# Optimization experiments

Measured on AMD Instinct MI355X. Metric: run time of the kernel, lower is better.

## Reference

```python
import math
import jax, jax.numpy as jnp
import numpy as np

WINDOW = 2  # LocalAttention default window_size
EPS = 1e-6


def _linear(x, W, b):
    return x @ W + b


def local_attention(x, Wq, bq, Wk, bk, Wv, bv):
    # x: [B, S, D]
    B, S, D = x.shape
    q = _linear(x, Wq, bq)
    k = _linear(x, Wk, bk)
    v = _linear(x, Wv, bv)
    idx = jnp.arange(S)
    # 0/1 banded mask -> softmax gives a dense row-stochastic matrix (faithful to source)
    mask = (jnp.abs(idx[:, None] - idx[None, :]) <= WINDOW).astype(x.dtype)  # [S, S]
    A = jax.nn.softmax(mask, axis=-1)  # [S, S]
    kk = jnp.einsum('st,btd->bsd', A, k)  # bmm(A, k)
    scores = jnp.einsum('bsd,btd->bst', q, kk) / math.sqrt(D)
    return jnp.einsum('bst,btd->bsd', jax.nn.softmax(scores, axis=-1), v)


def whole_norm(x, w, b):
    # LayerNorm with normalized_shape == full [B, S, D]: normalize over ALL elements
    mu = jnp.mean(x)
    var = jnp.mean(jnp.square(x - mu))
    return (x - mu) * jax.lax.rsqrt(var + EPS) * w + b


def ffn(x, W1, b1, W2, b2):
    return _linear(jax.nn.relu(_linear(x, W1, b1)), W2, b2)


def branch(feat, Wq, bq, Wk, bk, Wv, bv, W1, b1, W2, b2, nw, nb):
    out = local_attention(feat, Wq, bq, Wk, bk, Wv, bv)
    out = whole_norm(out + feat, nw, nb)
    out = ffn(out, W1, b1, W2, b2)
    return whole_norm(out + feat, nw, nb)


def _make_params(key, B, S, D):
    ks = jax.random.split(key, 5)
    s = 1.0 / math.sqrt(D)
    Wq = jax.random.normal(ks[0], (D, D), jnp.float32) * s
    Wk = jax.random.normal(ks[1], (D, D), jnp.float32) * s
    Wv = jax.random.normal(ks[2], (D, D), jnp.float32) * s
    W1 = jax.random.normal(ks[3], (D, 4 * D), jnp.float32) * s
    W2 = jax.random.normal(ks[4], (4 * D, D), jnp.float32) * (1.0 / math.sqrt(4 * D))
    return dict(Wq=Wq, bq=jnp.zeros((D,)), Wk=Wk, bk=jnp.zeros((D,)),
                Wv=Wv, bv=jnp.zeros((D,)), W1=W1, b1=jnp.zeros((4 * D,)),
                W2=W2, b2=jnp.zeros((D,)), nw=jnp.ones((B, S, D)), nb=jnp.zeros((B, S, D)))


def setup_inputs() -> dict:
    key = jax.random.key(0)
    k0, k1, k2, k3 = jax.random.split(key, 4)
    B, St, Dt = 8, 512, 1024
    Si, Di = 196, 768
    inp = {
        'text_feature': jax.random.normal(k0, (B, St, Dt), jnp.float32),
        'image_feature': jax.random.normal(k1, (B, Si, Di), jnp.float32),
    }
    tp = _make_params(k2, B, St, Dt)
    ip = _make_params(k3, B, Si, Di)
    for k, v in tp.items():
        inp['t_' + k] = v
    for k, v in ip.items():
        inp['i_' + k] = v
    return inp


def reference(text_feature, image_feature,
              t_Wq, t_bq, t_Wk, t_bk, t_Wv, t_bv, t_W1, t_b1, t_W2, t_b2, t_nw, t_nb,
              i_Wq, i_bq, i_Wk, i_bk, i_Wv, i_bv, i_W1, i_b1, i_W2, i_b2, i_nw, i_nb):
    image_out = branch(image_feature, i_Wq, i_bq, i_Wk, i_bk, i_Wv, i_bv,
                       i_W1, i_b1, i_W2, i_b2, i_nw, i_nb)
    text_out = branch(text_feature, t_Wq, t_bq, t_Wk, t_bk, t_Wv, t_bv,
                      t_W1, t_b1, t_W2, t_b2, t_nw, t_nb)
    return (text_out, image_out)
```

## Files before the change

kernel.cpp:

```cpp
#include <hip/hip_runtime.h>
#include <math.h>

typedef float  f32x4  __attribute__((ext_vector_type(4)));
typedef short  bf16x8 __attribute__((ext_vector_type(8)));

__device__ __forceinline__ unsigned short f2bf(float f) {
    union { float f; unsigned u; } v; v.f = f;
    unsigned u = v.u;
    return (unsigned short)((u + 0x7FFFu + ((u >> 16) & 1u)) >> 16);
}
__device__ __forceinline__ float bf2f(unsigned short u) {
    union { unsigned u; float f; } v; v.u = (unsigned)u << 16; return v.f;
}

#define GLOAD_LDS16(g, l)                                                      \
    __builtin_amdgcn_global_load_lds(                                          \
        (const __attribute__((address_space(1))) void*)(g),                    \
        (__attribute__((address_space(3))) void*)(l), 16, 0, 0)

template<int BM, int BN, bool OUT_BF16, bool RELU>
__global__ __launch_bounds__(256)
void gemm_bf16(const unsigned short* __restrict__ A,
               const unsigned short* __restrict__ BT,
               const float* __restrict__ bias, void* __restrict__ Cv,
               int M, int N, int K, int lda, int ldb, int ldc,
               long long sA, long long sB, long long sC, float alpha,
               int gx, int gy)
{
    constexpr int BK = 32;
    constexpr int WM = BM / 2, WN = BN / 2;
    constexpr int MR = WM / 16, NR = WN / 16;
    __shared__ unsigned short Asm[BM * BK];
    __shared__ unsigned short Bsm[BN * BK];

    A  += (long long)blockIdx.z * sA;
    BT += (long long)blockIdx.z * sB;
    char* Cb = (char*)Cv + (long long)blockIdx.z * sC * (OUT_BF16 ? 2 : 4);

    const int nwg = gx * gy;
    {
        int orig = blockIdx.x;
        int xcd = orig & 7, sidx = orig >> 3;
        int qq = nwg >> 3, rr = nwg & 7;
        int wg = (xcd < rr ? xcd * (qq + 1) : rr * (qq + 1) + (xcd - rr) * qq) + sidx;
        (void)wg;
        const int by = wg % gy;
        const int bx = wg / gy;
        __shared__ int rc[2];
        if (threadIdx.x == 0) { rc[0] = by * BM; rc[1] = bx * BN; }
        __syncthreads();
    }
    int orig = blockIdx.x;
    int xcd = orig & 7, sidx = orig >> 3;
    int qq = nwg >> 3, rr = nwg & 7;
    int wg = (xcd < rr ? xcd * (qq + 1) : rr * (qq + 1) + (xcd - rr) * qq) + sidx;
    const int row0 = (wg % gy) * BM;
    const int col0 = (wg / gy) * BN;

    const int tid  = threadIdx.x;
    const int lane = tid & 63;
    const int wave = tid >> 6;
    const int wr   = wave >> 1;
    const int wc   = wave & 1;

    const int srow = tid >> 2;
    const int skel = (tid & 3) * 8;

    f32x4 acc[MR][NR] = {};

    const int lrow = lane & 15;
    const int lk   = (lane >> 4) * 8;

    for (int k0 = 0; k0 < K; k0 += BK) {
        #pragma unroll
        for (int is = 0; is < BM / 64; ++is) {
            const unsigned short* g =
                A + (long long)(row0 + is * 64 + srow) * lda + (k0 + skel);
            GLOAD_LDS16(g, &Asm[(is * 64 + srow) * BK + skel]);
        }
        #pragma unroll
        for (int is = 0; is < BN / 64; ++is) {
            const unsigned short* g =
                BT + (long long)(col0 + is * 64 + srow) * ldb + (k0 + skel);
            GLOAD_LDS16(g, &Bsm[(is * 64 + srow) * BK + skel]);
        }
        __syncthreads();

        bf16x8 af[MR], bfr[NR];
        #pragma unroll
        for (int mf = 0; mf < MR; ++mf)
            af[mf] = *(const bf16x8*)&Asm[(wr * WM + mf * 16 + lrow) * BK + lk];
        #pragma unroll
        for (int nf = 0; nf < NR; ++nf)
            bfr[nf] = *(const bf16x8*)&Bsm[(wc * WN + nf * 16 + lrow) * BK + lk];
        #pragma unroll
        for (int mf = 0; mf < MR; ++mf)
            #pragma unroll
            for (int nf = 0; nf < NR; ++nf)
                acc[mf][nf] = __builtin_amdgcn_mfma_f32_16x16x32_bf16(
                    af[mf], bfr[nf], acc[mf][nf], 0, 0, 0);
        __syncthreads();
    }

    const int crow = (lane >> 4) * 4;
    const int ccol = lane & 15;
    #pragma unroll
    for (int mf = 0; mf < MR; ++mf) {
        int rbase = row0 + wr * WM + mf * 16 + crow;
        #pragma unroll
        for (int nf = 0; nf < NR; ++nf) {
            int c = col0 + wc * WN + nf * 16 + ccol;
            if (c >= N) continue;
            float bv = bias ? bias[c] : 0.f;
            #pragma unroll
            for (int j = 0; j < 4; ++j) {
                int r = rbase + j;
                if (r >= M) continue;
                float v = acc[mf][nf][j] * alpha + bv;
                if (RELU) v = fmaxf(v, 0.f);
                if (OUT_BF16)
                    ((unsigned short*)Cb)[(long long)r * ldc + c] = f2bf(v);
                else
                    ((float*)Cb)[(long long)r * ldc + c] = v;
            }
        }
    }
}

template<int BM, int BN>
static void gemm_t(bool outBf16, bool relu,
                   const unsigned short* A, const unsigned short* BT, const float* bias,
                   void* C, int M, int N, int K, int lda, int ldb, int ldc,
                   int batch, long long sA, long long sB, long long sC,
                   float alpha, hipStream_t st)
{
    int gx = (N + BN - 1) / BN, gy = (M + BM - 1) / BM;
    dim3 grid(gx * gy, 1, batch);
    if (outBf16) {
        if (relu) gemm_bf16<BM, BN, true , true ><<<grid, 256, 0, st>>>(A, BT, bias, C, M, N, K, lda, ldb, ldc, sA, sB, sC, alpha, gx, gy);
        else      gemm_bf16<BM, BN, true , false><<<grid, 256, 0, st>>>(A, BT, bias, C, M, N, K, lda, ldb, ldc, sA, sB, sC, alpha, gx, gy);
    } else {
        if (relu) gemm_bf16<BM, BN, false, true ><<<grid, 256, 0, st>>>(A, BT, bias, C, M, N, K, lda, ldb, ldc, sA, sB, sC, alpha, gx, gy);
        else      gemm_bf16<BM, BN, false, false><<<grid, 256, 0, st>>>(A, BT, bias, C, M, N, K, lda, ldb, ldc, sA, sB, sC, alpha, gx, gy);
    }
}

__global__ void splitk_reduce_kernel(const float4* __restrict__ part,
                                     const float4* __restrict__ bias,
                                     float4* __restrict__ out,
                                     long long n4, int N4, int nsplit, long long stride4)
{
    long long i = (long long)blockIdx.x * blockDim.x + threadIdx.x;
    long long gs = (long long)gridDim.x * blockDim.x;
    for (; i < n4; i += gs) {
        float4 a = part[i];
        for (int s = 1; s < nsplit; ++s) {
            float4 b = part[(long long)s * stride4 + i];
            a.x += b.x; a.y += b.y; a.z += b.z; a.w += b.w;
        }
        float4 bv = bias[(int)(i % N4)];
        a.x += bv.x; a.y += bv.y; a.z += bv.z; a.w += bv.w;
        out[i] = a;
    }
}

__global__ void cast_bf16_kernel(const float4* __restrict__ in,
                                 ushort4* __restrict__ out, long long n4)
{
    long long i = (long long)blockIdx.x * blockDim.x + threadIdx.x;
    long long stride = (long long)gridDim.x * blockDim.x;
    for (; i < n4; i += stride) {
        float4 v = in[i];
        ushort4 o;
        o.x = f2bf(v.x); o.y = f2bf(v.y); o.z = f2bf(v.z); o.w = f2bf(v.w);
        out[i] = o;
    }
}

__global__ void transpose_cast_kernel(const float* __restrict__ src,
                                      unsigned short* __restrict__ dst,
                                      int R, int C, int Rpad,
                                      long long sSrc, long long sDst)
{
    __shared__ float t[32][33];
    src += (long long)blockIdx.z * sSrc;
    dst += (long long)blockIdx.z * sDst;
    int r0 = blockIdx.x * 32, c0 = blockIdx.y * 32;
    int tx = threadIdx.x & 31, ty = threadIdx.x >> 5;
    #pragma unroll
    for (int i = 0; i < 32; i += 8) {
        int r = r0 + ty + i, c = c0 + tx;
        t[ty + i][tx] = (r < R && c < C) ? src[(long long)r * C + c] : 0.f;
    }
    __syncthreads();
    #pragma unroll
    for (int i = 0; i < 32; i += 8) {
        int c = c0 + ty + i, r = r0 + tx;
        if (c < C && r < Rpad)
            dst[(long long)c * Rpad + r] = f2bf(t[tx][ty + i]);
    }
}

__global__ void transpose_bf16_kernel(const unsigned short* __restrict__ src,
                                      unsigned short* __restrict__ dst,
                                      int R, int C, int Rpad, int ldS,
                                      long long sSrc, long long sDst)
{
    __shared__ unsigned short t[32][33];
    src += (long long)blockIdx.z * sSrc;
    dst += (long long)blockIdx.z * sDst;
    int r0 = blockIdx.x * 32, c0 = blockIdx.y * 32;
    int tx = threadIdx.x & 31, ty = threadIdx.x >> 5;
    #pragma unroll
    for (int i = 0; i < 32; i += 8) {
        int r = r0 + ty + i, c = c0 + tx;
        t[ty + i][tx] = (r < R && c < C) ? src[(long long)r * ldS + c] : (unsigned short)0;
    }
    __syncthreads();
    #pragma unroll
    for (int i = 0; i < 32; i += 8) {
        int c = c0 + ty + i, r = r0 + tx;
        if (c < C && r < Rpad)
            dst[(long long)c * Rpad + r] = t[tx][ty + i];
    }
}

#define KTOT_NCH 16
__global__ void ktot_partial_bf16(const unsigned short* __restrict__ k,
                                  float* __restrict__ part,
                                  int B, int S, int D, int ld)
{
    int bch = blockIdx.x;
    int b  = bch / KTOT_NCH;
    int ch = bch % KTOT_NCH;
    int d  = blockIdx.y * 256 + threadIdx.x;
    if (d >= D) return;
    int len = (S + KTOT_NCH - 1) / KTOT_NCH;
    int lo = ch * len;
    int hi = lo + len < S ? lo + len : S;
    const unsigned short* kp = k + ((long long)b * S + lo) * ld + d;
    float s = 0.f;
    for (int t = lo; t < hi; ++t, kp += ld) s += bf2f(*kp);
    part[(long long)bch * D + d] = s;
}

__global__ void ktot_finish_kernel(const float* __restrict__ part,
                                   float* __restrict__ ktot, int B, int D)
{
    int idx = blockIdx.x * blockDim.x + threadIdx.x;
    if (idx >= B * D) return;
    int b = idx / D, d = idx % D;
    float s = 0.f;
    #pragma unroll
    for (int ch = 0; ch < KTOT_NCH; ++ch)
        s += part[((long long)b * KTOT_NCH + ch) * D + d];
    ktot[idx] = s;
}

__global__ void kk_bf16_kernel(const unsigned short* __restrict__ k,
                               const float* __restrict__ ktot,
                               unsigned short* __restrict__ kk,
                               int B, int S, int D, int ld)
{
    long long idx = (long long)blockIdx.x * blockDim.x + threadIdx.x;
    int D4 = D >> 2;
    long long n4 = (long long)B * S * D4;
    if (idx >= n4) return;
    int d4 = (int)(idx % D4);
    long long bs = idx / D4;
    int s = (int)(bs % S);
    int b = (int)(bs / S);
    int lo = s - 2 > 0 ? s - 2 : 0;
    int hi = s + 2 < S - 1 ? s + 2 : S - 1;
    int c = hi - lo + 1;
    const float E = 2.718281828459045f;
    float Zinv = 1.f / ((float)(S - c) + E * (float)c);

    float w0 = 0.f, w1 = 0.f, w2 = 0.f, w3 = 0.f;
    const unsigned short* kp = k + ((long long)b * S + lo) * ld + d4 * 4;
    for (int t = lo; t <= hi; ++t, kp += ld) {
        ushort4 kv = *(const ushort4*)kp;
        w0 += bf2f(kv.x); w1 += bf2f(kv.y); w2 += bf2f(kv.z); w3 += bf2f(kv.w);
    }
    float4 tot = *((const float4*)(ktot + b * D) + d4);
    ushort4 o;
    o.x = f2bf((tot.x + (E - 1.f) * w0) * Zinv);
    o.y = f2bf((tot.y + (E - 1.f) * w1) * Zinv);
    o.z = f2bf((tot.z + (E - 1.f) * w2) * Zinv);
    o.w = f2bf((tot.w + (E - 1.f) * w3) * Zinv);
    ((ushort4*)(kk + ((long long)b * S + s) * D))[d4] = o;
}

__global__ void softmax_rows_bf16(const float* __restrict__ sc,
                                  unsigned short* __restrict__ P, int S, int Spad)
{
    long long row = blockIdx.x;
    const float* p = sc + row * (long long)Spad;
    unsigned short* o = P + row * (long long)Spad;
    int tid = threadIdx.x;
    __shared__ float red[256];

    float m = -INFINITY;
    for (int t = tid; t < S; t += 256) m = fmaxf(m, p[t]);
    red[tid] = m; __syncthreads();
    for (int s = 128; s > 0; s >>= 1) {
        if (tid < s) red[tid] = fmaxf(red[tid], red[tid + s]);
        __syncthreads();
    }
    m = red[0];
    __syncthreads();

    float sum = 0.f;
    for (int t = tid; t < S; t += 256) sum += __expf(p[t] - m);
    red[tid] = sum; __syncthreads();
    for (int s = 128; s > 0; s >>= 1) {
        if (tid < s) red[tid] += red[tid + s];
        __syncthreads();
    }
    float inv = 1.f / red[0];
    for (int t = tid; t < Spad; t += 256)
        o[t] = (t < S) ? f2bf(__expf(p[t] - m) * inv) : (unsigned short)0;
}

__global__ void stats_kernel(const float4* __restrict__ a, const float4* __restrict__ f,
                             double* __restrict__ part, long long n4)
{
    __shared__ double rs[256], rs2[256];
    int tid = threadIdx.x;
    long long i = (long long)blockIdx.x * blockDim.x + tid;
    long long stride = (long long)gridDim.x * blockDim.x;
    double s = 0.0, s2 = 0.0;
    for (; i < n4; i += stride) {
        float4 av = a[i], fv = f[i];
        float z0 = av.x + fv.x, z1 = av.y + fv.y, z2 = av.z + fv.z, z3 = av.w + fv.w;
        s  += (double)z0 + (double)z1 + (double)z2 + (double)z3;
        s2 += (double)z0 * z0 + (double)z1 * z1 + (double)z2 * z2 + (double)z3 * z3;
    }
    rs[tid] = s; rs2[tid] = s2; __syncthreads();
    for (int k = 128; k > 0; k >>= 1) {
        if (tid < k) { rs[tid] += rs[tid + k]; rs2[tid] += rs2[tid + k]; }
        __syncthreads();
    }
    if (tid == 0) { part[2 * blockIdx.x] = rs[0]; part[2 * blockIdx.x + 1] = rs2[0]; }
}

__global__ void finish_stats(const double* __restrict__ part, int npart,
                             float* __restrict__ stats, double n)
{
    __shared__ double rs[256], rs2[256];
    int tid = threadIdx.x;
    double s = 0.0, s2 = 0.0;
    for (int i = tid; i < npart; i += 256) { s += part[2 * i]; s2 += part[2 * i + 1]; }
    rs[tid] = s; rs2[tid] = s2; __syncthreads();
    for (int k = 128; k > 0; k >>= 1) {
        if (tid < k) { rs[tid] += rs[tid + k]; rs2[tid] += rs2[tid + k]; }
        __syncthreads();
    }
    if (tid == 0) {
        double mu  = rs[0] / n;
        double var = rs2[0] / n - mu * mu;
        stats[0] = (float)mu;
        stats[1] = (float)(1.0 / sqrt(var + 1e-6));
    }
}

template<bool OUT_BF16>
__global__ void norm_apply_kernel(const float4* __restrict__ a, const float4* __restrict__ f,
                                  const float4* __restrict__ nw, const float4* __restrict__ nb,
                                  const float* __restrict__ stats, void* __restrict__ out,
                                  long long n4)
{
    float mu = stats[0], rstd = stats[1];
    long long i = (long long)blockIdx.x * blockDim.x + threadIdx.x;
    long long stride = (long long)gridDim.x * blockDim.x;
    for (; i < n4; i += stride) {
        float4 av = a[i], fv = f[i], wv = nw[i], bv = nb[i];
        float o0 = (av.x + fv.x - mu) * rstd * wv.x + bv.x;
        float o1 = (av.y + fv.y - mu) * rstd * wv.y + bv.y;
        float o2 = (av.z + fv.z - mu) * rstd * wv.z + bv.z;
        float o3 = (av.w + fv.w - mu) * rstd * wv.w + bv.w;
        if (OUT_BF16) {
            ushort4 o; o.x = f2bf(o0); o.y = f2bf(o1); o.z = f2bf(o2); o.w = f2bf(o3);
            ((ushort4*)out)[i] = o;
        } else {
            float4 o = {o0, o1, o2, o3};
            ((float4*)out)[i] = o;
        }
    }
}

struct Bufs {
    unsigned short *xb, *qkv, *kkb, *vT, *P, *h, *WqkvT, *W1T, *W2T;
    float *f32buf, *bqkv, *ktot, *ktot_part, *stats;
    double *part;
};

static void run_branch(const float* x, const float* const* w, bool big,
                       float* out, int B, int S, int D, const Bufs& wsb, hipStream_t st)
{
    const float *Wq = w[0], *bq = w[1], *Wk = w[2], *bk = w[3], *Wv = w[4], *bv = w[5];
    const float *W1 = w[6], *b1 = w[7], *W2 = w[8], *b2 = w[9], *nw = w[10], *nb = w[11];

    const int Spad = (S + 31) & ~31;
    const long long M = (long long)B * S;
    const long long n = M * D;
    const long long n4 = n / 4;
    const float inv_sqrt_d = (float)(1.0 / sqrt((double)D));
    const int D3 = 3 * D, D4 = 4 * D;

    unsigned short* y1b = wsb.kkb;
    float* scores = (float*)wsb.h;
    float* splitbuf = (float*)wsb.qkv;

    cast_bf16_kernel<<<1024, 256, 0, st>>>((const float4*)x, (ushort4*)wsb.xb, n4);
    transpose_cast_kernel<<<dim3((D + 31) / 32, (D + 31) / 32, 1), 256, 0, st>>>(Wq, wsb.WqkvT,            D, D, D, 0, 0);
    transpose_cast_kernel<<<dim3((D + 31) / 32, (D + 31) / 32, 1), 256, 0, st>>>(Wk, wsb.WqkvT + (long long)D * D,     D, D, D, 0, 0);
    transpose_cast_kernel<<<dim3((D + 31) / 32, (D + 31) / 32, 1), 256, 0, st>>>(Wv, wsb.WqkvT + 2LL * D * D, D, D, D, 0, 0);
    transpose_cast_kernel<<<dim3((D + 31) / 32, (D4 + 31) / 32, 1), 256, 0, st>>>(W1, wsb.W1T, D, D4, D, 0, 0);
    transpose_cast_kernel<<<dim3((D4 + 31) / 32, (D + 31) / 32, 1), 256, 0, st>>>(W2, wsb.W2T, D4, D, D4, 0, 0);
    hipMemcpyAsync(wsb.bqkv,         bq, D * sizeof(float), hipMemcpyDeviceToDevice, st);
    hipMemcpyAsync(wsb.bqkv + D,     bk, D * sizeof(float), hipMemcpyDeviceToDevice, st);
    hipMemcpyAsync(wsb.bqkv + 2 * D, bv, D * sizeof(float), hipMemcpyDeviceToDevice, st);

    if (big)
        gemm_t<128, 128>(true, false, wsb.xb, wsb.WqkvT, wsb.bqkv, wsb.qkv,
                         (int)M, D3, D, D, D, D3, 1, 0, 0, 0, 1.f, st);
    else
        gemm_t<128, 64>(true, false, wsb.xb, wsb.WqkvT, wsb.bqkv, wsb.qkv,
                        (int)M, D3, D, D, D, D3, 1, 0, 0, 0, 1.f, st);

    const unsigned short* kcol = wsb.qkv + D;
    ktot_partial_bf16<<<dim3(B * KTOT_NCH, (D + 255) / 256), 256, 0, st>>>(kcol, wsb.ktot_part, B, S, D, D3);
    ktot_finish_kernel<<<(B * D + 255) / 256, 256, 0, st>>>(wsb.ktot_part, wsb.ktot, B, D);
    kk_bf16_kernel<<<(int)((n4 + 255) / 256), 256, 0, st>>>(kcol, wsb.ktot, wsb.kkb, B, S, D, D3);

    transpose_bf16_kernel<<<dim3((Spad + 31) / 32, (D + 31) / 32, B), 256, 0, st>>>(
        wsb.qkv + 2 * D, wsb.vT, S, D, Spad, D3, (long long)S * D3, (long long)D * Spad);

    gemm_t<64, 64>(false, false, wsb.qkv, wsb.kkb, nullptr, scores, S, S, D, D3, D, Spad,
                   B, (long long)S * D3, (long long)S * D, (long long)S * Spad, inv_sqrt_d, st);
    softmax_rows_bf16<<<(int)M, 256, 0, st>>>(scores, wsb.P, S, Spad);

    gemm_t<128, 64>(false, false, wsb.P, wsb.vT, nullptr, wsb.f32buf, S, D, Spad, Spad, Spad, D,
                    B, (long long)S * Spad, (long long)D * Spad, (long long)S * D, 1.f, st);

    stats_kernel<<<1024, 256, 0, st>>>((const float4*)wsb.f32buf, (const float4*)x, wsb.part, n4);
    finish_stats<<<1, 256, 0, st>>>(wsb.part, 1024, wsb.stats, (double)n);
    norm_apply_kernel<true><<<2048, 256, 0, st>>>((const float4*)wsb.f32buf, (const float4*)x,
        (const float4*)nw, (const float4*)nb, wsb.stats, y1b, n4);

    if (big)
        gemm_t<128, 128>(true, true, y1b, wsb.W1T, b1, wsb.h, (int)M, D4, D, D, D, D4, 1, 0, 0, 0, 1.f, st);
    else
        gemm_t<128, 64>(true, true, y1b, wsb.W1T, b1, wsb.h, (int)M, D4, D, D, D, D4, 1, 0, 0, 0, 1.f, st);

    {
        int nsplit = big ? 2 : 4;
        int Ksp = D4 / nsplit;
        gemm_t<128, 64>(false, false, wsb.h, wsb.W2T, nullptr, splitbuf,
                        (int)M, D, Ksp, D4, D4, D,
                        nsplit, Ksp, Ksp, M * D, 1.f, st);
        splitk_reduce_kernel<<<2048, 256, 0, st>>>((const float4*)splitbuf, (const float4*)b2,
                                                   (float4*)wsb.f32buf, n4, D / 4, nsplit, n4);
    }

    stats_kernel<<<1024, 256, 0, st>>>((const float4*)wsb.f32buf, (const float4*)x, wsb.part, n4);
    finish_stats<<<1, 256, 0, st>>>(wsb.part, 1024, wsb.stats, (double)n);
    norm_apply_kernel<false><<<2048, 256, 0, st>>>((const float4*)wsb.f32buf, (const float4*)x,
        (const float4*)nw, (const float4*)nb, wsb.stats, out, n4);
}

extern "C" void kernel_launch(void* const* d_in, const int* in_sizes, int n_in,
                              void* d_out, int out_size, void* d_ws, size_t ws_size,
                              hipStream_t stream)
{
    const float* text  = (const float*)d_in[0];
    const float* image = (const float*)d_in[1];
    const float* tw[12];
    const float* iw[12];
    for (int i = 0; i < 12; ++i) tw[i] = (const float*)d_in[2 + i];
    for (int i = 0; i < 12; ++i) iw[i] = (const float*)d_in[14 + i];

    float* out_text = (float*)d_out;
    float* out_img  = out_text + 8LL * 512 * 1024;

    char* p = (char*)d_ws;
    auto alloc = [&](long long bytes) {
        char* r = p;
        p += (bytes + 255) & ~255LL;
        return r;
    };
    const long long MD  = 4096LL * 1024;
    const long long BDS = 8LL * 1024 * 512;
    const long long SS  = 8LL * 512 * 512;
    Bufs b;
    b.xb      = (unsigned short*)alloc(MD * 2);
    b.qkv     = (unsigned short*)alloc(MD * 3 * 2);
    b.kkb     = (unsigned short*)alloc(MD * 2);
    b.vT      = (unsigned short*)alloc(BDS * 2);
    b.P       = (unsigned short*)alloc(SS * 2);
    b.h       = (unsigned short*)alloc(MD * 4 * 2);
    b.WqkvT   = (unsigned short*)alloc(3LL * 1024 * 1024 * 2);
    b.W1T     = (unsigned short*)alloc(4096LL * 1024 * 2);
    b.W2T     = (unsigned short*)alloc(4096LL * 1024 * 2);
    b.f32buf  = (float*)alloc(MD * 4);
    b.bqkv    = (float*)alloc(3LL * 1024 * 4);
    b.ktot    = (float*)alloc(8192LL * 4);
    b.ktot_part = (float*)alloc(8192LL * KTOT_NCH * 4);
    b.part    = (double*)alloc(2048LL * 8);
    b.stats   = (float*)alloc(256);

    run_branch(text,  tw, true,  out_text, 8, 512, 1024, b, stream);
    run_branch(image, iw, false, out_img,  8, 196, 768,  b, stream);
}
```

Baseline: 522.4 us.

## Add double-buffered 8-wave GEMM for projections and fuse split-K reduce with norm stats

Adds a new GEMM kernel with 512 threads (8 waves in a 2x4 arrangement), double-buffered LDS tiles and a single barrier per K step, so global-to-LDS loads for the next tile overlap MFMA work on the current one. It is used for the QKV, FFN1 and FFN2 projections with larger tiles on the big branch. The split-K reduction now also adds the residual and accumulates the whole-tensor sum and sum of squares, which removes one full read pass before the final norm. The costs are higher LDS use per block and different occupancy, plus a barrier-free window between staging the next tile and reading the current one.

```diff
diff --git a/kernel.cpp b/kernel.cpp
--- a/kernel.cpp
+++ b/kernel.cpp
@@ -18,38 +18,26 @@
         (const __attribute__((address_space(1))) void*)(g),                    \
         (__attribute__((address_space(3))) void*)(l), 16, 0, 0)
 
-template<int BM, int BN, bool OUT_BF16, bool RELU>
-__global__ __launch_bounds__(256)
-void gemm_bf16(const unsigned short* __restrict__ A,
-               const unsigned short* __restrict__ BT,
-               const float* __restrict__ bias, void* __restrict__ Cv,
-               int M, int N, int K, int lda, int ldb, int ldc,
-               long long sA, long long sB, long long sC, float alpha,
-               int gx, int gy)
+template<int MR, int NR, bool OUT_BF16, bool RELU>
+__global__ __launch_bounds__(512, 2)
+void gemm2_bf16(const unsigned short* __restrict__ A,
+                const unsigned short* __restrict__ BT,
+                const float* __restrict__ bias, void* __restrict__ Cv,
+                int M, int N, int K, int lda, int ldb, int ldc,
+                long long sA, long long sB, long long sC, float alpha,
+                int gx, int gy)
 {
     constexpr int BK = 32;
-    constexpr int WM = BM / 2, WN = BN / 2;
-    constexpr int MR = WM / 16, NR = WN / 16;
-    __shared__ unsigned short Asm[BM * BK];
-    __shared__ unsigned short Bsm[BN * BK];
+    constexpr int WM = MR * 16, WN = NR * 16;
+    constexpr int BM = 2 * WM, BN = 4 * WN;
+    __shared__ unsigned short Asm[2][BM * BK];
+    __shared__ unsigned short Bsm[2][BN * BK];
 
     A  += (long long)blockIdx.z * sA;
     BT += (long long)blockIdx.z * sB;
     char* Cb = (char*)Cv + (long long)blockIdx.z * sC * (OUT_BF16 ? 2 : 4);
 
     const int nwg = gx * gy;
-    {
-        int orig = blockIdx.x;
-        int xcd = orig & 7, sidx = orig >> 3;
-        int qq = nwg >> 3, rr = nwg & 7;
-        int wg = (xcd < rr ? xcd * (qq + 1) : rr * (qq + 1) + (xcd - rr) * qq) + sidx;
-        (void)wg;
-        const int by = wg % gy;
-        const int bx = wg / gy;
-        __shared__ int rc[2];
-        if (threadIdx.x == 0) { rc[0] = by * BM; rc[1] = bx * BN; }
-        __syncthreads();
-    }
     int orig = blockIdx.x;
     int xcd = orig & 7, sidx = orig >> 3;
     int qq = nwg >> 3, rr = nwg & 7;
@@ -60,46 +48,51 @@
     const int tid  = threadIdx.x;
     const int lane = tid & 63;
     const int wave = tid >> 6;
-    const int wr   = wave >> 1;
-    const int wc   = wave & 1;
+    const int wr   = wave >> 2;
+    const int wc   = wave & 3;
 
     const int srow = tid >> 2;
     const int skel = (tid & 3) * 8;
 
-    f32x4 acc[MR][NR] = {};
-
     const int lrow = lane & 15;
     const int lk   = (lane >> 4) * 8;
 
-    for (int k0 = 0; k0 < K; k0 += BK) {
-        #pragma unroll
-        for (int is = 0; is < BM / 64; ++is) {
-            const unsigned short* g =
-                A + (long long)(row0 + is * 64 + srow) * lda + (k0 + skel);
-            GLOAD_LDS16(g, &Asm[(is * 64 + srow) * BK + skel]);
-        }
-        #pragma unroll
-        for (int is = 0; is < BN / 64; ++is) {
-            const unsigned short* g =
-                BT + (long long)(col0 + is * 64 + srow) * ldb + (k0 + skel);
-            GLOAD_LDS16(g, &Bsm[(is * 64 + srow) * BK + skel]);
-        }
-        __syncthreads();
+    f32x4 acc[MR][NR] = {};
+
+    auto stage = [&](int buf, int k0) {
+        #pragma unroll
+        for (int is = 0; is < BM / 128; ++is)
+            GLOAD_LDS16(A + (long long)(row0 + is * 128 + srow) * lda + (k0 + skel),
+                        &Asm[buf][(is * 128 + srow) * BK + skel]);
+        #pragma unroll
+        for (int is = 0; is < BN / 128; ++is)
+            GLOAD_LDS16(BT + (long long)(col0 + is * 128 + srow) * ldb + (k0 + skel),
+                        &Bsm[buf][(is * 128 + srow) * BK + skel]);
+    };
+
+    const int nt = K / BK;
+    stage(0, 0);
+    __syncthreads();
+    int cur = 0;
+    for (int t = 0; t < nt; ++t) {
+        if (t + 1 < nt) stage(cur ^ 1, (t + 1) * BK);
 
         bf16x8 af[MR], bfr[NR];
         #pragma unroll
         for (int mf = 0; mf < MR; ++mf)
-            af[mf] = *(const bf16x8*)&Asm[(wr * WM + mf * 16 + lrow) * BK + lk];
+            af[mf] = *(const bf16x8*)&Asm[cur][(wr * WM + mf * 16 + lrow) * BK + lk];
         #pragma unroll
         for (int nf = 0; nf < NR; ++nf)
-            bfr[nf] = *(const bf16x8*)&Bsm[(wc * WN + nf * 16 + lrow) * BK + lk];
+            bfr[nf] = *(const bf16x8*)&Bsm[cur][(wc * WN + nf * 16 + lrow) * BK + lk];
         #pragma unroll
         for (int mf = 0; mf < MR; ++mf)
             #pragma unroll
             for (int nf = 0; nf < NR; ++nf)
                 acc[mf][nf] = __builtin_amdgcn_mfma_f32_16x16x32_bf16(
                     af[mf], bfr[nf], acc[mf][nf], 0, 0, 0);
-        __syncthreads();
+
+        __syncthreads();
+        cur ^= 1;
     }
 
     const int crow = (lane >> 4) * 4;
@@ -127,8 +120,119 @@
     }
 }
 
+template<int MR, int NR>
+static void gemm2_t(bool outBf16, bool relu,
+                    const unsigned short* A, const unsigned short* BT, const float* bias,
+                    void* C, int M, int N, int K, int lda, int ldb, int ldc,
+                    int batch, long long sA, long long sB, long long sC,
+                    float alpha, hipStream_t st)
+{
+    const int BM = 2 * MR * 16, BN = 4 * NR * 16;
+    int gx = (N + BN - 1) / BN, gy = (M + BM - 1) / BM;
+    dim3 grid(gx * gy, 1, batch);
+    if (outBf16) {
+        if (relu) gemm2_bf16<MR, NR, true , true ><<<grid, 512, 0, st>>>(A, BT, bias, C, M, N, K, lda, ldb, ldc, sA, sB, sC, alpha, gx, gy);
+        else      gemm2_bf16<MR, NR, true , false><<<grid, 512, 0, st>>>(A, BT, bias, C, M, N, K, lda, ldb, ldc, sA, sB, sC, alpha, gx, gy);
+    } else {
+        if (relu) gemm2_bf16<MR, NR, false, true ><<<grid, 512, 0, st>>>(A, BT, bias, C, M, N, K, lda, ldb, ldc, sA, sB, sC, alpha, gx, gy);
+        else      gemm2_bf16<MR, NR, false, false><<<grid, 512, 0, st>>>(A, BT, bias, C, M, N, K, lda, ldb, ldc, sA, sB, sC, alpha, gx, gy);
+    }
+}
+
+template<int BM, int BN, bool OUT_BF16>
+__global__ __launch_bounds__(256)
+void gemm_bf16(const unsigned short* __restrict__ A,
+               const unsigned short* __restrict__ BT,
+               const float* __restrict__ bias, void* __restrict__ Cv,
+               int M, int N, int K, int lda, int ldb, int ldc,
+               long long sA, long long sB, long long sC, float alpha,
+               int gx, int gy)
+{
+    constexpr int BK = 32;
+    constexpr int WM = BM / 2, WN = BN / 2;
+    constexpr int MR = WM / 16, NR = WN / 16;
+    __shared__ unsigned short Asm[BM * BK];
+    __shared__ unsigned short Bsm[BN * BK];
+
+    A  += (long long)blockIdx.z * sA;
+    BT += (long long)blockIdx.z * sB;
+    char* Cb = (char*)Cv + (long long)blockIdx.z * sC * (OUT_BF16 ? 2 : 4);
+
+    const int nwg = gx * gy;
+    int orig = blockIdx.x;
+    int xcd = orig & 7, sidx = orig >> 3;
+    int qq = nwg >> 3, rr = nwg & 7;
+    int wg = (xcd < rr ? xcd * (qq + 1) : rr * (qq + 1) + (xcd - rr) * qq) + sidx;
+    const int row0 = (wg % gy) * BM;
+    const int col0 = (wg / gy) * BN;
+
+    const int tid  = threadIdx.x;
+    const int lane = tid & 63;
+    const int wave = tid >> 6;
+    const int wr   = wave >> 1;
+    const int wc   = wave & 1;
+
+    const int srow = tid >> 2;
+    const int skel = (tid & 3) * 8;
+
+    f32x4 acc[MR][NR] = {};
+
+    const int lrow = lane & 15;
+    const int lk   = (lane >> 4) * 8;
+
+    for (int k0 = 0; k0 < K; k0 += BK) {
+        #pragma unroll
+        for (int is = 0; is < BM / 64; ++is)
+            GLOAD_LDS16(A + (long long)(row0 + is * 64 + srow) * lda + (k0 + skel),
+                        &Asm[(is * 64 + srow) * BK + skel]);
+        #pragma unroll
+        for (int is = 0; is < BN / 64; ++is)
+            GLOAD_LDS16(BT + (long long)(col0 + is * 64 + srow) * ldb + (k0 + skel),
+                        &Bsm[(is * 64 + srow) * BK + skel]);
+        __syncthreads();
+
+        bf16x8 af[MR], bfr[NR];
+        #pragma unroll
+        for (int mf = 0; mf < MR; ++mf)
+            af[mf] = *(const bf16x8*)&Asm[(wr * WM + mf * 16 + lrow) * BK + lk];
+        #pragma unroll
+        for (int nf = 0; nf < NR; ++nf)
+            bfr[nf] = *(const bf16x8*)&Bsm[(wc * WN + nf * 16 + lrow) * BK + lk];
+        #pragma unroll
+        for (int mf = 0; mf < MR; ++mf)
+            #pragma unroll
+            for (int nf = 0; nf < NR; ++nf)
+                acc[mf][nf] = __builtin_amdgcn_mfma_f32_16x16x32_bf16(
+                    af[mf], bfr[nf], acc[mf][nf], 0, 0, 0);
+        __syncthreads();
+    }
+
+    const int crow = (lane >> 4) * 4;
+    const int ccol = lane & 15;
+    #pragma unroll
+    for (int mf = 0; mf < MR; ++mf) {
+        int rbase = row0 + wr * WM + mf * 16 + crow;
+        #pragma unroll
+        for (int nf = 0; nf < NR; ++nf) {
+            int c = col0 + wc * WN + nf * 16 + ccol;
+            if (c >= N) continue;
+            float bv = bias ? bias[c] : 0.f;
+            #pragma unroll
+            for (int j = 0; j < 4; ++j) {
+                int r = rbase + j;
+                if (r >= M) continue;
+                float v = acc[mf][nf][j] * alpha + bv;
+                if (OUT_BF16)
+                    ((unsigned short*)Cb)[(long long)r * ldc + c] = f2bf(v);
+                else
+                    ((float*)Cb)[(long long)r * ldc + c] = v;
+            }
+        }
+    }
+}
+
 template<int BM, int BN>
-static void gemm_t(bool outBf16, bool relu,
+static void gemm_t(bool outBf16,
                    const unsigned short* A, const unsigned short* BT, const float* bias,
                    void* C, int M, int N, int K, int lda, int ldb, int ldc,
                    int batch, long long sA, long long sB, long long sC,
@@ -136,31 +240,61 @@
 {
     int gx = (N + BN - 1) / BN, gy = (M + BM - 1) / BM;
     dim3 grid(gx * gy, 1, batch);
-    if (outBf16) {
-        if (relu) gemm_bf16<BM, BN, true , true ><<<grid, 256, 0, st>>>(A, BT, bias, C, M, N, K, lda, ldb, ldc, sA, sB, sC, alpha, gx, gy);
-        else      gemm_bf16<BM, BN, true , false><<<grid, 256, 0, st>>>(A, BT, bias, C, M, N, K, lda, ldb, ldc, sA, sB, sC, alpha, gx, gy);
-    } else {
-        if (relu) gemm_bf16<BM, BN, false, true ><<<grid, 256, 0, st>>>(A, BT, bias, C, M, N, K, lda, ldb, ldc, sA, sB, sC, alpha, gx, gy);
-        else      gemm_bf16<BM, BN, false, false><<<grid, 256, 0, st>>>(A, BT, bias, C, M, N, K, lda, ldb, ldc, sA, sB, sC, alpha, gx, gy);
-    }
-}
-
-__global__ void splitk_reduce_kernel(const float4* __restrict__ part,
-                                     const float4* __restrict__ bias,
-                                     float4* __restrict__ out,
-                                     long long n4, int N4, int nsplit, long long stride4)
-{
-    long long i = (long long)blockIdx.x * blockDim.x + threadIdx.x;
+    if (outBf16)
+        gemm_bf16<BM, BN, true ><<<grid, 256, 0, st>>>(A, BT, bias, C, M, N, K, lda, ldb, ldc, sA, sB, sC, alpha, gx, gy);
+    else
+        gemm_bf16<BM, BN, false><<<grid, 256, 0, st>>>(A, BT, bias, C, M, N, K, lda, ldb, ldc, sA, sB, sC, alpha, gx, gy);
+}
+
+__global__ void splitk_stats_kernel(const float4* __restrict__ part,
+                                    const float4* __restrict__ bias,
+                                    const float4* __restrict__ x,
+                                    float4* __restrict__ z,
+                                    double* __restrict__ dpart,
+                                    long long n4, int N4, int nsplit, long long stride4)
+{
+    __shared__ double rs[256], rs2[256];
+    int tid = threadIdx.x;
+    long long i = (long long)blockIdx.x * blockDim.x + tid;
     long long gs = (long long)gridDim.x * blockDim.x;
+    double s = 0.0, s2 = 0.0;
     for (; i < n4; i += gs) {
         float4 a = part[i];
-        for (int s = 1; s < nsplit; ++s) {
-            float4 b = part[(long long)s * stride4 + i];
+        for (int sp = 1; sp < nsplit; ++sp) {
+            float4 b = part[(long long)sp * stride4 + i];
             a.x += b.x; a.y += b.y; a.z += b.z; a.w += b.w;
         }
         float4 bv = bias[(int)(i % N4)];
-        a.x += bv.x; a.y += bv.y; a.z += bv.z; a.w += bv.w;
-        out[i] = a;
+        float4 xv = x[i];
+        a.x += bv.x + xv.x; a.y += bv.y + xv.y; a.z += bv.z + xv.z; a.w += bv.w + xv.w;
+        z[i] = a;
+        s  += (double)a.x + (double)a.y + (double)a.z + (double)a.w;
+        s2 += (double)a.x * a.x + (double)a.y * a.y + (double)a.z * a.z + (double)a.w * a.w;
+    }
+    rs[tid] = s; rs2[tid] = s2; __syncthreads();
+    for (int k = 128; k > 0; k >>= 1) {
+        if (tid < k) { rs[tid] += rs[tid + k]; rs2[tid] += rs2[tid + k]; }
+        __syncthreads();
+    }
+    if (tid == 0) { dpart[2 * blockIdx.x] = rs[0]; dpart[2 * blockIdx.x + 1] = rs2[0]; }
+}
+
+__global__ void norm_apply_z_kernel(const float4* __restrict__ z,
+                                    const float4* __restrict__ nw, const float4* __restrict__ nb,
+                                    const float* __restrict__ stats, float4* __restrict__ out,
+                                    long long n4)
+{
+    float mu = stats[0], rstd = stats[1];
+    long long i = (long long)blockIdx.x * blockDim.x + threadIdx.x;
+    long long stride = (long long)gridDim.x * blockDim.x;
+    for (; i < n4; i += stride) {
+        float4 zv = z[i], wv = nw[i], bv = nb[i];
+        float4 o;
+        o.x = (zv.x - mu) * rstd * wv.x + bv.x;
+        o.y = (zv.y - mu) * rstd * wv.y + bv.y;
+        o.z = (zv.z - mu) * rstd * wv.z + bv.z;
+        o.w = (zv.w - mu) * rstd * wv.w + bv.w;
+        out[i] = o;
     }
 }
 
@@ -364,10 +498,9 @@
     }
 }
 
-template<bool OUT_BF16>
 __global__ void norm_apply_kernel(const float4* __restrict__ a, const float4* __restrict__ f,
                                   const float4* __restrict__ nw, const float4* __restrict__ nb,
-                                  const float* __restrict__ stats, void* __restrict__ out,
+                                  const float* __restrict__ stats, ushort4* __restrict__ out,
                                   long long n4)
 {
     float mu = stats[0], rstd = stats[1];
@@ -375,17 +508,12 @@
     long long stride = (long long)gridDim.x * blockDim.x;
     for (; i < n4; i += stride) {
         float4 av = a[i], fv = f[i], wv = nw[i], bv = nb[i];
-        float o0 = (av.x + fv.x - mu) * rstd * wv.x + bv.x;
-        float o1 = (av.y + fv.y - mu) * rstd * wv.y + bv.y;
-        float o2 = (av.z + fv.z - mu) * rstd * wv.z + bv.z;
-        float o3 = (av.w + fv.w - mu) * rstd * wv.w + bv.w;
-        if (OUT_BF16) {
-            ushort4 o; o.x = f2bf(o0); o.y = f2bf(o1); o.z = f2bf(o2); o.w = f2bf(o3);
-            ((ushort4*)out)[i] = o;
-        } else {
-            float4 o = {o0, o1, o2, o3};
-            ((float4*)out)[i] = o;
-        }
+        ushort4 o;
+        o.x = f2bf((av.x + fv.x - mu) * rstd * wv.x + bv.x);
+        o.y = f2bf((av.y + fv.y - mu) * rstd * wv.y + bv.y);
+        o.z = f2bf((av.z + fv.z - mu) * rstd * wv.z + bv.z);
+        o.w = f2bf((av.w + fv.w - mu) * rstd * wv.w + bv.w);
+        out[i] = o;
     }
 }
 
@@ -413,8 +541,8 @@
     float* splitbuf = (float*)wsb.qkv;
 
     cast_bf16_kernel<<<1024, 256, 0, st>>>((const float4*)x, (ushort4*)wsb.xb, n4);
-    transpose_cast_kernel<<<dim3((D + 31) / 32, (D + 31) / 32, 1), 256, 0, st>>>(Wq, wsb.WqkvT,            D, D, D, 0, 0);
-    transpose_cast_kernel<<<dim3((D + 31) / 32, (D + 31) / 32, 1), 256, 0, st>>>(Wk, wsb.WqkvT + (long long)D * D,     D, D, D, 0, 0);
+    transpose_cast_kernel<<<dim3((D + 31) / 32, (D + 31) / 32, 1), 256, 0, st>>>(Wq, wsb.WqkvT,               D, D, D, 0, 0);
+    transpose_cast_kernel<<<dim3((D + 31) / 32, (D + 31) / 32, 1), 256, 0, st>>>(Wk, wsb.WqkvT + (long long)D * D, D, D, D, 0, 0);
     transpose_cast_kernel<<<dim3((D + 31) / 32, (D + 31) / 32, 1), 256, 0, st>>>(Wv, wsb.WqkvT + 2LL * D * D, D, D, D, 0, 0);
     transpose_cast_kernel<<<dim3((D + 31) / 32, (D4 + 31) / 32, 1), 256, 0, st>>>(W1, wsb.W1T, D, D4, D, 0, 0);
     transpose_cast_kernel<<<dim3((D4 + 31) / 32, (D + 31) / 32, 1), 256, 0, st>>>(W2, wsb.W2T, D4, D, D4, 0, 0);
@@ -423,11 +551,11 @@
     hipMemcpyAsync(wsb.bqkv + 2 * D, bv, D * sizeof(float), hipMemcpyDeviceToDevice, st);
 
     if (big)
-        gemm_t<128, 128>(true, false, wsb.xb, wsb.WqkvT, wsb.bqkv, wsb.qkv,
-                         (int)M, D3, D, D, D, D3, 1, 0, 0, 0, 1.f, st);
+        gemm2_t<8, 2>(true, false, wsb.xb, wsb.WqkvT, wsb.bqkv, wsb.qkv,
+                      (int)M, D3, D, D, D, D3, 1, 0, 0, 0, 1.f, st);
     else
-        gemm_t<128, 64>(true, false, wsb.xb, wsb.WqkvT, wsb.bqkv, wsb.qkv,
-                        (int)M, D3, D, D, D, D3, 1, 0, 0, 0, 1.f, st);
+        gemm2_t<4, 2>(true, false, wsb.xb, wsb.WqkvT, wsb.bqkv, wsb.qkv,
+                      (int)M, D3, D, D, D, D3, 1, 0, 0, 0, 1.f, st);
 
     const unsigned short* kcol = wsb.qkv + D;
     ktot_partial_bf16<<<dim3(B * KTOT_NCH, (D + 255) / 256), 256, 0, st>>>(kcol, wsb.ktot_part, B, S, D, D3);
@@ -437,37 +565,41 @@
     transpose_bf16_kernel<<<dim3((Spad + 31) / 32, (D + 31) / 32, B), 256, 0, st>>>(
         wsb.qkv + 2 * D, wsb.vT, S, D, Spad, D3, (long long)S * D3, (long long)D * Spad);
 
-    gemm_t<64, 64>(false, false, wsb.qkv, wsb.kkb, nullptr, scores, S, S, D, D3, D, Spad,
+    gemm_t<64, 64>(false, wsb.qkv, wsb.kkb, nullptr, scores, S, S, D, D3, D, Spad,
                    B, (long long)S * D3, (long long)S * D, (long long)S * Spad, inv_sqrt_d, st);
     softmax_rows_bf16<<<(int)M, 256, 0, st>>>(scores, wsb.P, S, Spad);
 
-    gemm_t<128, 64>(false, false, wsb.P, wsb.vT, nullptr, wsb.f32buf, S, D, Spad, Spad, Spad, D,
+    gemm_t<128, 64>(false, wsb.P, wsb.vT, nullptr, wsb.f32buf, S, D, Spad, Spad, Spad, D,
                     B, (long long)S * Spad, (long long)D * Spad, (long long)S * D, 1.f, st);
 
     stats_kernel<<<1024, 256, 0, st>>>((const float4*)wsb.f32buf, (const float4*)x, wsb.part, n4);
     finish_stats<<<1, 256, 0, st>>>(wsb.part, 1024, wsb.stats, (double)n);
-    norm_apply_kernel<true><<<2048, 256, 0, st>>>((const float4*)wsb.f32buf, (const float4*)x,
-        (const float4*)nw, (const float4*)nb, wsb.stats, y1b, n4);
+    norm_apply_kernel<<<2048, 256, 0, st>>>((const float4*)wsb.f32buf, (const float4*)x,
+        (const float4*)nw, (const float4*)nb, wsb.stats, (ushort4*)y1b, n4);
 
     if (big)
-        gemm_t<128, 128>(true, true, y1b, wsb.W1T, b1, wsb.h, (int)M, D4, D, D, D, D4, 1, 0, 0, 0, 1.f, st);
+        gemm2_t<8, 4>(true, true, y1b, wsb.W1T, b1, wsb.h, (int)M, D4, D, D, D, D4, 1, 0, 0, 0, 1.f, st);
     else
-        gemm_t<128, 64>(true, true, y1b, wsb.W1T, b1, wsb.h, (int)M, D4, D, D, D, D4, 1, 0, 0, 0, 1.f, st);
+        gemm2_t<4, 2>(true, true, y1b, wsb.W1T, b1, wsb.h, (int)M, D4, D, D, D, D4, 1, 0, 0, 0, 1.f, st);
 
     {
         int nsplit = big ? 2 : 4;
         int Ksp = D4 / nsplit;
-        gemm_t<128, 64>(false, false, wsb.h, wsb.W2T, nullptr, splitbuf,
-                        (int)M, D, Ksp, D4, D4, D,
-                        nsplit, Ksp, Ksp, M * D, 1.f, st);
-        splitk_reduce_kernel<<<2048, 256, 0, st>>>((const float4*)splitbuf, (const float4*)b2,
-                                                   (float4*)wsb.f32buf, n4, D / 4, nsplit, n4);
-    }
-
-    stats_kernel<<<1024, 256, 0, st>>>((const float4*)wsb.f32buf, (const float4*)x, wsb.part, n4);
-    finish_stats<<<1, 256, 0, st>>>(wsb.part, 1024, wsb.stats, (double)n);
-    norm_apply_kernel<false><<<2048, 256, 0, st>>>((const float4*)wsb.f32buf, (const float4*)x,
-        (const float4*)nw, (const float4*)nb, wsb.stats, out, n4);
+        if (big)
+            gemm2_t<8, 2>(false, false, wsb.h, wsb.W2T, nullptr, splitbuf,
+                          (int)M, D, Ksp, D4, D4, D,
+                          nsplit, Ksp, Ksp, M * D, 1.f, st);
+        else
+            gemm2_t<4, 2>(false, false, wsb.h, wsb.W2T, nullptr, splitbuf,
+                          (int)M, D, Ksp, D4, D4, D,
+                          nsplit, Ksp, Ksp, M * D, 1.f, st);
+        splitk_stats_kernel<<<1024, 256, 0, st>>>((const float4*)splitbuf, (const float4*)b2,
+                                                  (const float4*)x, (float4*)wsb.f32buf,
+                                                  wsb.part, n4, D / 4, nsplit, n4);
+        finish_stats<<<1, 256, 0, st>>>(wsb.part, 1024, wsb.stats, (double)n);
+        norm_apply_z_kernel<<<2048, 256, 0, st>>>((const float4*)wsb.f32buf,
+            (const float4*)nw, (const float4*)nb, wsb.stats, (float4*)out, n4);
+    }
 }
 
 extern "C" void kernel_launch(void* const* d_in, const int* in_sizes, int n_in,
```

After: 503.3 us (median of 3 runs). 1.04x faster.
